# Kernel tuning notes

Measured on AMD Instinct MI355X. Metric: run time of the kernel, lower is better.

The kernel has to match this reference:

```python
import jax, jax.numpy as jnp
import numpy as np

DIM, HEADS, DHEAD = 256, 8, 64
INNER = HEADS * DHEAD
EPS = 1e-5


def _ln(x, g, b):
    m = x.mean(-1, keepdims=True)
    v = ((x - m) ** 2).mean(-1, keepdims=True)
    return (x - m) / jnp.sqrt(v + EPS) * g + b


def setup_inputs() -> dict:
    key = jax.random.key(0)
    ks = jax.random.split(key, 24)
    b, n, Q, K = 1, 6, 900, 1408
    d = DIM
    s = lambda fan_in: 1.0 / np.sqrt(fan_in)
    inp = {
        "k_g": jax.random.normal(ks[0], (b, n, K, d), jnp.float32),
        "q_g": jax.random.normal(ks[1], (b, n, Q, d), jnp.float32),
        "k_a": jax.random.normal(ks[2], (b, n, K, d), jnp.float32),
        "q_a": jax.random.normal(ks[3], (b, Q, d), jnp.float32),
        "v": jax.random.normal(ks[4], (b, n, K, d), jnp.float32),
        "mask": jax.random.randint(ks[5], (b, n, K), 0, 2).astype(bool),
        # projections (stored as (in, out))
        "W_qg": jax.random.uniform(ks[6], (d, INNER), jnp.float32, -s(d), s(d)),
        "b_qg": jnp.zeros((INNER,), jnp.float32),
        "W_kg": jax.random.uniform(ks[7], (d, INNER), jnp.float32, -s(d), s(d)),
        "b_kg": jnp.zeros((INNER,), jnp.float32),
        "W_qa": jax.random.uniform(ks[8], (d, INNER), jnp.float32, -s(d), s(d)),
        "b_qa": jnp.zeros((INNER,), jnp.float32),
        "W_ka": jax.random.uniform(ks[9], (d, INNER), jnp.float32, -s(d), s(d)),
        "b_ka": jnp.zeros((INNER,), jnp.float32),
        "W_v": jax.random.uniform(ks[10], (d, INNER), jnp.float32, -s(d), s(d)),
        "b_v": jnp.zeros((INNER,), jnp.float32),
        "W_o": jax.random.uniform(ks[11], (INNER, d), jnp.float32, -s(INNER), s(INNER)),
        "b_o": jnp.zeros((d,), jnp.float32),
        "ln1_g": jnp.ones((d,), jnp.float32),
        "ln1_b": jnp.zeros((d,), jnp.float32),
        "W_m1": jax.random.uniform(ks[12], (d, 2 * d), jnp.float32, -s(d), s(d)),
        "b_m1": jnp.zeros((2 * d,), jnp.float32),
        "W_m2": jax.random.uniform(ks[13], (2 * d, d), jnp.float32, -s(2 * d), s(2 * d)),
        "b_m2": jnp.zeros((d,), jnp.float32),
        "ln2_g": jnp.ones((d,), jnp.float32),
        "ln2_b": jnp.zeros((d,), jnp.float32),
        "scale_g": jnp.full((HEADS,), DHEAD ** -0.5, jnp.float32),
        "scale_a": jnp.full((HEADS,), DHEAD ** -0.5, jnp.float32),
    }
    return inp


def reference(k_g, q_g, k_a, q_a, v, mask,
              W_qg, b_qg, W_kg, b_kg, W_qa, b_qa, W_ka, b_ka, W_v, b_v,
              W_o, b_o, ln1_g, ln1_b, W_m1, b_m1, W_m2, b_m2, ln2_g, ln2_b,
              scale_g, scale_a):
    b, n, Q, _ = q_g.shape
    K = k_g.shape[2]
    h, dh = HEADS, DHEAD
    skip = q_a

    def split(x):  # (..., h*dh) -> (b, h, ..., dh)
        return jnp.moveaxis(x.reshape(x.shape[:-1] + (h, dh)), -2, 1)

    kg = split(k_g @ W_kg + b_kg)          # (b, h, n, K, dh)
    qg = split(q_g @ W_qg + b_qg)          # (b, h, n, Q, dh)
    ka = split(k_a @ W_ka + b_ka)          # (b, h, n, K, dh)
    qa = split(q_a @ W_qa + b_qa)          # (b, h, Q, dh)
    vv = split(v @ W_v + b_v)              # (b, h, n, K, dh)

    dot_g = jnp.einsum('bhnqd,bhnkd->bhnqk', qg, kg)
    dot_a = jnp.einsum('bhqd,bhnkd->bhnqk', qa, ka)
    sg = scale_g[None, :, None, None, None]
    sa = scale_a[None, :, None, None, None]
    dot = sg * dot_g + sa * dot_a
    dot = jnp.where(mask[:, None, :, None, :], -jnp.inf, dot)

    # softmax jointly over (n, K)
    dot = dot.transpose(0, 1, 3, 2, 4).reshape(b, h, Q, n * K)
    att = jax.nn.softmax(dot, axis=-1)
    vflat = vv.reshape(b, h, n * K, dh)
    a = jnp.einsum('bhqk,bhkd->bhqd', att, vflat)
    a = a.transpose(0, 2, 1, 3).reshape(b, Q, h * dh)

    z = a @ W_o + b_o + skip
    z = _ln(z, ln1_g, ln1_b)
    z = z + (jax.nn.gelu(z @ W_m1 + b_m1, approximate=False) @ W_m2 + b_m2)
    z = _ln(z, ln2_g, ln2_b)
    return z
```

## Files before the change

### kernel.cpp

```cpp
#include <hip/hip_runtime.h>
#include <stdint.h>

typedef unsigned short u16;
typedef _Float16 half8 __attribute__((ext_vector_type(8)));
typedef _Float16 half4 __attribute__((ext_vector_type(4)));
typedef _Float16 half2 __attribute__((ext_vector_type(2)));
typedef float f32x4 __attribute__((ext_vector_type(4)));

__device__ __forceinline__ u16 f2h(float f) {
    _Float16 h = (_Float16)f; u16 u; __builtin_memcpy(&u, &h, 2); return u;
}
__device__ __forceinline__ float h2f(u16 u) {
    _Float16 h; __builtin_memcpy(&h, &u, 2); return (float)h;
}

template<int CTRL>
__device__ __forceinline__ float dppf(float x) {
    return __builtin_bit_cast(float,
        __builtin_amdgcn_update_dpp(0, __builtin_bit_cast(int, x), CTRL, 0xF, 0xF, false));
}
__device__ __forceinline__ float sum16(float x) {
    x += dppf<0xB1>(x);
    x += dppf<0x4E>(x);
    x += dppf<0x124>(x);
    x += dppf<0x128>(x);
    return x;
}

__global__ __launch_bounds__(256) void prep_kernel(
    const float* __restrict__ W_qg, const float* __restrict__ W_kg,
    const float* __restrict__ W_qa, const float* __restrict__ W_ka,
    const float* __restrict__ W_v,  const float* __restrict__ W_o,
    const float* __restrict__ W_m1, const float* __restrict__ W_m2,
    u16* __restrict__ T_qg, u16* __restrict__ T_kg, u16* __restrict__ T_qa,
    u16* __restrict__ T_ka, u16* __restrict__ T_v,  u16* __restrict__ T_o,
    u16* __restrict__ T_m1, u16* __restrict__ T_m2,
    const float* __restrict__ scale_g, const float* __restrict__ scale_a,
    const float* __restrict__ b_kg, const float* __restrict__ b_ka,
    float* __restrict__ bkg_s, float* __restrict__ bka_s,
    const int* __restrict__ mask, int* __restrict__ mflag)
{
    const int z = blockIdx.z;
    const int tid = threadIdx.x;
    if (z == 8) {
        if (blockIdx.y != 0) return;
        if (blockIdx.x == 0) {
            __shared__ int f;
            if (tid == 0) f = 0;
            __syncthreads();
            int local = 0;
            for (int i = tid; i < 2112; i += 256) { int vv = mask[i]; if (vv & ~1) local = 1; }
            if (local) atomicOr(&f, 1);
            __syncthreads();
            if (tid == 0) *mflag = f;
        } else if (blockIdx.x == 1) {
            for (int j = tid; j < 512; j += 256) {
                bkg_s[j] = b_kg[j] * scale_g[j >> 6];
                bka_s[j] = b_ka[j] * scale_a[j >> 6];
            }
        }
        return;
    }
    const int K = (z == 5 || z == 7) ? 512 : 256;
    const int N = (z == 5 || z == 7) ? 256 : 512;
    const int k0 = blockIdx.x * 64, n0 = blockIdx.y * 64;
    if (k0 >= K || n0 >= N) return;
    const float* W = z==0?W_qg: z==1?W_kg: z==2?W_qa: z==3?W_ka: z==4?W_v: z==5?W_o: z==6?W_m1: W_m2;
    u16* D        = z==0?T_qg: z==1?T_kg: z==2?T_qa: z==3?T_ka: z==4?T_v: z==5?T_o: z==6?T_m1: T_m2;
    const float* scp = z==1 ? scale_g : z==3 ? scale_a : nullptr;

    __shared__ u16 T[64][80];
    const int cr = tid >> 4, cc = (tid & 15) * 4;
    const float sc = scp ? scp[(n0 + cc) >> 6] : 1.0f;
    #pragma unroll
    for (int i = 0; i < 4; ++i) {
        const int r = cr + i * 16;
        const float4 vv = *(const float4*)(W + (size_t)(k0 + r) * N + n0 + cc);
        T[cc + 0][r] = f2h(vv.x * sc);
        T[cc + 1][r] = f2h(vv.y * sc);
        T[cc + 2][r] = f2h(vv.z * sc);
        T[cc + 3][r] = f2h(vv.w * sc);
    }
    __syncthreads();
    const int nr = tid >> 2, part = (tid & 3) * 16;
    u16* drow = D + (size_t)(n0 + nr) * K + k0 + part;
    *(half8*)(drow)     = *(const half8*)&T[nr][part];
    *(half8*)(drow + 8) = *(const half8*)&T[nr][part + 8];
}

__global__ __launch_bounds__(256, 4) void proj_all(
    const float* __restrict__ k_g, const float* __restrict__ k_a,
    const float* __restrict__ v,   const float* __restrict__ q_g,
    const float* __restrict__ q_a,
    const u16* __restrict__ T_kg, const u16* __restrict__ T_ka,
    const u16* __restrict__ T_v,  const u16* __restrict__ T_qg,
    const u16* __restrict__ T_qa,
    const float* __restrict__ bkg_s, const float* __restrict__ bka_s,
    const float* __restrict__ b_v,   const float* __restrict__ b_qg,
    const float* __restrict__ b_qa,
    u16* __restrict__ qcat, u16* __restrict__ kcat, u16* __restrict__ vt)
{
    __shared__ u16 Ws[256 * 36];

    int bx = blockIdx.x;
    int mode, M;
    const float* X; const u16* Wt; const float* bias; u16* out;
    if (bx < 132)      { mode = 2; M = 8448; X = k_g; Wt = T_kg; bias = bkg_s; out = kcat; }
    else if (bx < 264) { mode = 3; M = 8448; X = k_a; Wt = T_ka; bias = bka_s; out = kcat; bx -= 132; }
    else if (bx < 396) { mode = 4; M = 8448; X = v;   Wt = T_v;  bias = b_v;   out = vt;   bx -= 264; }
    else if (bx < 481) { mode = 0; M = 5400; X = q_g; Wt = T_qg; bias = b_qg;  out = qcat; bx -= 396; }
    else               { mode = 1; M = 900;  X = q_a; Wt = T_qa; bias = b_qa;  out = qcat; bx -= 481; }
    const int rows_per_n = (mode == 0) ? 900 : 1408;

    const int tid = threadIdx.x;
    const int w = tid >> 6, lane = tid & 63;
    const int l15 = lane & 15, quad = lane >> 4;
    const int m0 = bx * 64;
    const int nbase = blockIdx.y * 256;
    const int row = m0 + w * 16 + l15;

    const float* xrow = X + (size_t)(row < M ? row : 0) * 256 + quad * 8;
    const u16* wcol = Wt + ((size_t)(nbase + tid) << 8);

    f32x4 o[4][4];
    #pragma unroll
    for (int nt = 0; nt < 4; ++nt)
        #pragma unroll
        for (int t = 0; t < 4; ++t) { o[nt][t][0]=0.f; o[nt][t][1]=0.f; o[nt][t][2]=0.f; o[nt][t][3]=0.f; }

    for (int k0 = 0; k0 < 8; ++k0) {
        {
            const uint4 w0 = *(const uint4*)(wcol + k0 * 32 + 0);
            const uint4 w1 = *(const uint4*)(wcol + k0 * 32 + 8);
            const uint4 w2 = *(const uint4*)(wcol + k0 * 32 + 16);
            const uint4 w3 = *(const uint4*)(wcol + k0 * 32 + 24);
            *(uint4*)&Ws[tid * 36 + 0]  = w0;
            *(uint4*)&Ws[tid * 36 + 8]  = w1;
            *(uint4*)&Ws[tid * 36 + 16] = w2;
            *(uint4*)&Ws[tid * 36 + 24] = w3;
        }
        __syncthreads();

        const float4 a0 = *(const float4*)(xrow + k0 * 32);
        const float4 a1 = *(const float4*)(xrow + k0 * 32 + 4);
        half8 af;
        af[0]=(_Float16)a0.x; af[1]=(_Float16)a0.y; af[2]=(_Float16)a0.z; af[3]=(_Float16)a0.w;
        af[4]=(_Float16)a1.x; af[5]=(_Float16)a1.y; af[6]=(_Float16)a1.z; af[7]=(_Float16)a1.w;

        #pragma unroll
        for (int nt = 0; nt < 4; ++nt)
            #pragma unroll
            for (int t = 0; t < 4; ++t) {
                const half8 bf = *(const half8*)&Ws[(nt * 64 + t * 16 + l15) * 36 + quad * 8];
                o[nt][t] = __builtin_amdgcn_mfma_f32_16x16x32_f16(af, bf, o[nt][t], 0, 0, 0);
            }
        __syncthreads();
    }

    #pragma unroll
    for (int nt = 0; nt < 4; ++nt) {
        const int n0 = nbase + nt * 64;
        const int hh = n0 >> 6;
        float bj[4];
        #pragma unroll
        for (int t = 0; t < 4; ++t) bj[t] = bias[n0 + t * 16 + l15];

        if (mode == 4) {
            const int gr0 = m0 + w * 16 + quad * 4;
            if (gr0 < M) {
                const int nI = gr0 / rows_per_n;
                const int rr = gr0 - nI * rows_per_n;
                u16* vb = out + (size_t)(hh * 6 + nI) * 64 * 1408;
                #pragma unroll
                for (int t = 0; t < 4; ++t) {
                    const int d = t * 16 + l15;
                    ushort4 pk;
                    pk.x = f2h(o[nt][t][0] + bj[t]);
                    pk.y = f2h(o[nt][t][1] + bj[t]);
                    pk.z = f2h(o[nt][t][2] + bj[t]);
                    pk.w = f2h(o[nt][t][3] + bj[t]);
                    *(ushort4*)&vb[(size_t)d * 1408 + rr] = pk;
                }
            }
        } else if (mode == 1) {
            #pragma unroll
            for (int r = 0; r < 4; ++r) {
                const int gr = m0 + w * 16 + quad * 4 + r;
                if (gr < M) {
                    for (int nb = 0; nb < 6; ++nb) {
                        u16* qb = out + (((size_t)(hh * 6 + nb) * 900 + gr) << 7) + 64;
                        #pragma unroll
                        for (int t = 0; t < 4; ++t)
                            qb[t * 16 + l15] = f2h(o[nt][t][r] + bj[t]);
                    }
                }
            }
        } else {
            const size_t kdim = (mode == 0) ? 900 : 1408;
            const int doff = (mode == 3) ? 64 : 0;
            #pragma unroll
            for (int r = 0; r < 4; ++r) {
                const int gr = m0 + w * 16 + quad * 4 + r;
                if (gr < M) {
                    const int nI = gr / rows_per_n;
                    const int rr = gr - nI * rows_per_n;
                    u16* ob = out + (((size_t)(hh * 6 + nI) * kdim + rr) << 7) + doff;
                    #pragma unroll
                    for (int t = 0; t < 4; ++t)
                        ob[t * 16 + l15] = f2h(o[nt][t][r] + bj[t]);
                }
            }
        }
    }
}

__global__ __launch_bounds__(256, 2) void attn_kernel(
    const u16* __restrict__ qcat, const u16* __restrict__ kcat,
    const u16* __restrict__ vt, const void* __restrict__ maskp,
    const int* __restrict__ mflag,
    u16* __restrict__ Opart, float* __restrict__ lpart)
{
    __shared__ __align__(16) u16 SMEM[64 * 136 + 64 * 72];
    __shared__ float Mb[64];
    u16* Ks = SMEM;
    u16* Vs = SMEM + 64 * 136;

    const int flat = blockIdx.x;
    const int hn_i = (flat & 7) + 8 * ((flat >> 3) % 6);
    const int qt = flat / 48;
    const int n = hn_i - (hn_i / 6) * 6;

    const int q0 = qt * 64;
    const int tid = threadIdx.x;
    const int w = tid >> 6, lane = tid & 63;
    const int l15 = lane & 15, quad = lane >> 4;
    const bool m8 = (*mflag != 0);
    const size_t hn = (size_t)hn_i;

    const u16* kbase = kcat + ((hn * 1408) << 7);
    const u16* vbase = vt + hn * 64 * 1408;
    const unsigned char* mB = (const unsigned char*)maskp;
    const int* mI = (const int*)maskp;
    const int mko = n * 1408;

    const int krow_s = tid >> 4;
    const int kcol_s = (tid & 15) * 8;
    const int vrow_s = tid >> 3;
    const int vcol_s = (tid & 7) * 8;

    half8 qf[4][4];
    #pragma unroll
    for (int qq = 0; qq < 4; ++qq) {
        const int gq = q0 + qq * 16 + l15;
        if (gq < 900) {
            const u16* qrow = qcat + ((hn * 900 + gq) << 7) + quad * 8;
            #pragma unroll
            for (int k0 = 0; k0 < 4; ++k0)
                qf[qq][k0] = *(const half8*)(qrow + k0 * 32);
        } else {
            #pragma unroll
            for (int k0 = 0; k0 < 4; ++k0)
                #pragma unroll
                for (int j = 0; j < 8; ++j) qf[qq][k0][j] = (_Float16)0.0f;
        }
    }

    f32x4 o[4][4];
    float lacc[4];
    #pragma unroll
    for (int dt = 0; dt < 4; ++dt)
        #pragma unroll
        for (int qq = 0; qq < 4; ++qq) { o[dt][qq][0]=0.f; o[dt][qq][1]=0.f; o[dt][qq][2]=0.f; o[dt][qq][3]=0.f; }
    #pragma unroll
    for (int qq = 0; qq < 4; ++qq) lacc[qq] = 0.f;

    uint4 kA, kB, kC, kD, vA, vB;
    float mreg = 0.0f;
    {
        kA = *(const uint4*)(kbase + ((size_t)( 0 + krow_s) << 7) + kcol_s);
        kB = *(const uint4*)(kbase + ((size_t)(16 + krow_s) << 7) + kcol_s);
        kC = *(const uint4*)(kbase + ((size_t)(32 + krow_s) << 7) + kcol_s);
        kD = *(const uint4*)(kbase + ((size_t)(48 + krow_s) << 7) + kcol_s);
        vA = *(const uint4*)(vbase + (size_t)(vrow_s)      * 1408 + vcol_s);
        vB = *(const uint4*)(vbase + (size_t)(32 + vrow_s) * 1408 + vcol_s);
        if (tid < 64) {
            const int ki = mko + tid;
            const int mv = m8 ? (int)mB[ki] : mI[ki];
            mreg = mv ? -1e30f : 0.0f;
        }
    }

    for (int cc = 0; cc < 22; ++cc) {
        *(uint4*)&Ks[( 0 + krow_s) * 136 + kcol_s] = kA;
        *(uint4*)&Ks[(16 + krow_s) * 136 + kcol_s] = kB;
        *(uint4*)&Ks[(32 + krow_s) * 136 + kcol_s] = kC;
        *(uint4*)&Ks[(48 + krow_s) * 136 + kcol_s] = kD;
        *(uint4*)&Vs[(vrow_s)      * 72 + vcol_s] = vA;
        *(uint4*)&Vs[(32 + vrow_s) * 72 + vcol_s] = vB;
        if (tid < 64) Mb[tid] = mreg;
        __syncthreads();

        if (cc < 21) {
            const int k0n = (cc + 1) * 64;
            kA = *(const uint4*)(kbase + ((size_t)(k0n +  0 + krow_s) << 7) + kcol_s);
            kB = *(const uint4*)(kbase + ((size_t)(k0n + 16 + krow_s) << 7) + kcol_s);
            kC = *(const uint4*)(kbase + ((size_t)(k0n + 32 + krow_s) << 7) + kcol_s);
            kD = *(const uint4*)(kbase + ((size_t)(k0n + 48 + krow_s) << 7) + kcol_s);
            vA = *(const uint4*)(vbase + (size_t)(vrow_s)      * 1408 + k0n + vcol_s);
            vB = *(const uint4*)(vbase + (size_t)(32 + vrow_s) * 1408 + k0n + vcol_s);
            if (tid < 64) {
                const int ki = mko + k0n + tid;
                const int mv = m8 ? (int)mB[ki] : mI[ki];
                mreg = mv ? -1e30f : 0.0f;
            }
        }

        float mb[4];
        #pragma unroll
        for (int r = 0; r < 4; ++r) mb[r] = Mb[w * 16 + quad * 4 + r];

        f32x4 s[4];
        #pragma unroll
        for (int qq = 0; qq < 4; ++qq) { s[qq][0]=mb[0]; s[qq][1]=mb[1]; s[qq][2]=mb[2]; s[qq][3]=mb[3]; }

        #pragma unroll
        for (int k0 = 0; k0 < 4; ++k0) {
            const half8 kf = *(const half8*)&Ks[(w * 16 + l15) * 136 + k0 * 32 + quad * 8];
            #pragma unroll
            for (int qq = 0; qq < 4; ++qq)
                s[qq] = __builtin_amdgcn_mfma_f32_16x16x32_f16(kf, qf[qq][k0], s[qq], 0, 0, 0);
        }

        half4 pf[4];
        #pragma unroll
        for (int qq = 0; qq < 4; ++qq) {
            const float p0 = __expf(s[qq][0]);
            const float p1 = __expf(s[qq][1]);
            const float p2 = __expf(s[qq][2]);
            const float p3 = __expf(s[qq][3]);
            lacc[qq] += (p0 + p1) + (p2 + p3);
            const half2 lo = __builtin_bit_cast(half2, __builtin_amdgcn_cvt_pkrtz(p0, p1));
            const half2 hi = __builtin_bit_cast(half2, __builtin_amdgcn_cvt_pkrtz(p2, p3));
            half4 pk; pk[0]=lo[0]; pk[1]=lo[1]; pk[2]=hi[0]; pk[3]=hi[1];
            pf[qq] = pk;
        }

        #pragma unroll
        for (int dt = 0; dt < 4; ++dt) {
            const half4 vf = *(const half4*)&Vs[(dt * 16 + l15) * 72 + w * 16 + quad * 4];
            #pragma unroll
            for (int qq = 0; qq < 4; ++qq)
                o[dt][qq] = __builtin_amdgcn_mfma_f32_16x16x16f16(vf, pf[qq], o[dt][qq], 0, 0, 0);
        }
        __syncthreads();
    }

    __syncthreads();
    float* Red = (float*)SMEM;
    float* Lp  = (float*)(SMEM + 64 * 136);

    #pragma unroll
    for (int qq = 0; qq < 4; ++qq)
        Lp[(w * 4 + quad) * 64 + qq * 16 + l15] = lacc[qq];
    #pragma unroll
    for (int qq = 0; qq < 4; ++qq)
        #pragma unroll
        for (int r = 0; r < 4; ++r)
            Red[(w * 16 + quad * 4 + r) * 68 + qq * 16 + l15] = o[0][qq][r];
    __syncthreads();

    if (tid < 64) {
        float l = 0.f;
        #pragma unroll
        for (int i = 0; i < 16; ++i) l += Lp[i * 64 + tid];
        if (q0 + tid < 900) lpart[hn_i * 900 + q0 + tid] = l;
    }

    const int dloc = tid & 15, qgrp = tid >> 4;
    #pragma unroll
    for (int dt = 0; dt < 4; ++dt) {
        #pragma unroll
        for (int i = 0; i < 4; ++i) {
            const int q = qgrp * 4 + i;
            const float sum = Red[( 0 + dloc) * 68 + q] + Red[(16 + dloc) * 68 + q]
                            + Red[(32 + dloc) * 68 + q] + Red[(48 + dloc) * 68 + q];
            const int gq = q0 + q;
            if (gq < 900)
                Opart[((size_t)hn_i * 900 + gq) * 64 + dt * 16 + dloc] = f2h(sum);
        }
        if (dt < 3) {
            __syncthreads();
            #pragma unroll
            for (int qq = 0; qq < 4; ++qq)
                #pragma unroll
                for (int r = 0; r < 4; ++r)
                    Red[(w * 16 + quad * 4 + r) * 68 + qq * 16 + l15] = o[dt + 1][qq][r];
            __syncthreads();
        }
    }
}

__global__ __launch_bounds__(256) void combine_kernel(
    const u16* __restrict__ Opart, const float* __restrict__ lpart,
    u16* __restrict__ a16)
{
    const int g = blockIdx.x * 256 + threadIdx.x;
    const int h = g / 14400;
    const int r = g - h * 14400;
    const int q = r >> 4;
    const int d4 = (r & 15) * 4;
    float l = 0.f;
    float o0 = 0.f, o1 = 0.f, o2 = 0.f, o3 = 0.f;
    #pragma unroll
    for (int s = 0; s < 6; ++s) {
        const int p = h * 6 + s;
        l += lpart[p * 900 + q];
        const ushort4 t = *(const ushort4*)&Opart[((size_t)p * 900 + q) * 64 + d4];
        o0 += h2f(t.x); o1 += h2f(t.y); o2 += h2f(t.z); o3 += h2f(t.w);
    }
    const float inv = 1.0f / fmaxf(l, 1e-30f);
    ushort4 outp;
    outp.x = f2h(o0 * inv); outp.y = f2h(o1 * inv);
    outp.z = f2h(o2 * inv); outp.w = f2h(o3 * inv);
    *(ushort4*)&a16[(size_t)q * 512 + h * 64 + d4] = outp;
}

__global__ __launch_bounds__(256) void epi_mega(
    const u16* __restrict__ a16, const u16* __restrict__ T_o,
    const u16* __restrict__ T_m1, const u16* __restrict__ T_m2,
    const float* __restrict__ b_o, const float* __restrict__ q_a,
    const float* __restrict__ ln1_g, const float* __restrict__ ln1_b,
    const float* __restrict__ b_m1, const float* __restrict__ b_m2,
    const float* __restrict__ ln2_g, const float* __restrict__ ln2_b,
    float* __restrict__ outf)
{
    __shared__ u16 Z1[16][264];
    __shared__ u16 H[16][520];
    __shared__ float Ssum[4][16];
    __shared__ float Ssq[4][16];

    const int tid = threadIdx.x;
    const int w = tid >> 6, lane = tid & 63;
    const int l15 = lane & 15, quad = lane >> 4;
    const int m0 = blockIdx.x * 4;

    {
        const int ar = m0 + l15;
        const u16* arow = a16 + (size_t)(ar < 900 ? ar : 899) * 512 + quad * 8;

        f32x4 acc[4];
        #pragma unroll
        for (int t = 0; t < 4; ++t) { acc[t][0]=0.f; acc[t][1]=0.f; acc[t][2]=0.f; acc[t][3]=0.f; }

        #pragma unroll
        for (int k0 = 0; k0 < 16; ++k0) {
            const half8 af = *(const half8*)(arow + k0 * 32);
            #pragma unroll
            for (int t = 0; t < 4; ++t) {
                const int nn = w * 64 + t * 16 + l15;
                const half8 bf = *(const half8*)(T_o + (size_t)nn * 512 + k0 * 32 + quad * 8);
                acc[t] = __builtin_amdgcn_mfma_f32_16x16x32_f16(af, bf, acc[t], 0, 0, 0);
            }
        }

        float vals[4][4];
        #pragma unroll
        for (int r = 0; r < 4; ++r) {
            const int row = m0 + quad * 4 + r;
            const int rows = row < 900 ? row : 899;
            float s = 0.f, sq = 0.f;
            #pragma unroll
            for (int t = 0; t < 4; ++t) {
                const int col = w * 64 + t * 16 + l15;
                const float x = acc[t][r] + b_o[col] + q_a[(size_t)rows * 256 + col];
                vals[r][t] = x; s += x; sq += x * x;
            }
            s = sum16(s); sq = sum16(sq);
            if (l15 == 0) { Ssum[w][quad * 4 + r] = s; Ssq[w][quad * 4 + r] = sq; }
        }
        __syncthreads();

        #pragma unroll
        for (int r = 0; r < 4; ++r) {
            const int rl = quad * 4 + r;
            const float st = Ssum[0][rl] + Ssum[1][rl] + Ssum[2][rl] + Ssum[3][rl];
            const float qt = Ssq[0][rl] + Ssq[1][rl] + Ssq[2][rl] + Ssq[3][rl];
            const float mean = st * (1.0f / 256.0f);
            const float var  = qt * (1.0f / 256.0f) - mean * mean;
            const float inv  = rsqrtf(var + 1e-5f);
            #pragma unroll
            for (int t = 0; t < 4; ++t) {
                const int col = w * 64 + t * 16 + l15;
                const float z = (vals[r][t] - mean) * inv * ln1_g[col] + ln1_b[col];
                Z1[rl][col] = f2h(z);
            }
        }
        __syncthreads();
    }

    {
        f32x4 acc[8];
        #pragma unroll
        for (int t = 0; t < 8; ++t) { acc[t][0]=0.f; acc[t][1]=0.f; acc[t][2]=0.f; acc[t][3]=0.f; }

        #pragma unroll
        for (int k0 = 0; k0 < 8; ++k0) {
            const half8 af = *(const half8*)&Z1[l15][k0 * 32 + quad * 8];
            #pragma unroll
            for (int t = 0; t < 8; ++t) {
                const int nn = w * 128 + t * 16 + l15;
                const half8 bf = *(const half8*)(T_m1 + (size_t)nn * 256 + k0 * 32 + quad * 8);
                acc[t] = __builtin_amdgcn_mfma_f32_16x16x32_f16(af, bf, acc[t], 0, 0, 0);
            }
        }

        #pragma unroll
        for (int r = 0; r < 4; ++r) {
            const int rl = quad * 4 + r;
            #pragma unroll
            for (int t = 0; t < 8; ++t) {
                const int col = w * 128 + t * 16 + l15;
                const float x = acc[t][r] + b_m1[col];
                H[rl][col] = f2h(0.5f * x * (1.0f + erff(x * 0.70710678118654752f)));
            }
        }
        __syncthreads();
    }

    {
        f32x4 acc[4];
        #pragma unroll
        for (int t = 0; t < 4; ++t) { acc[t][0]=0.f; acc[t][1]=0.f; acc[t][2]=0.f; acc[t][3]=0.f; }

        #pragma unroll
        for (int k0 = 0; k0 < 16; ++k0) {
            const half8 af = *(const half8*)&H[l15][k0 * 32 + quad * 8];
            #pragma unroll
            for (int t = 0; t < 4; ++t) {
                const int nn = w * 64 + t * 16 + l15;
                const half8 bf = *(const half8*)(T_m2 + (size_t)nn * 512 + k0 * 32 + quad * 8);
                acc[t] = __builtin_amdgcn_mfma_f32_16x16x32_f16(af, bf, acc[t], 0, 0, 0);
            }
        }

        float vals[4][4];
        #pragma unroll
        for (int r = 0; r < 4; ++r) {
            const int rl = quad * 4 + r;
            float s = 0.f, sq = 0.f;
            #pragma unroll
            for (int t = 0; t < 4; ++t) {
                const int col = w * 64 + t * 16 + l15;
                const float x = acc[t][r] + b_m2[col] + h2f(Z1[rl][col]);
                vals[r][t] = x; s += x; sq += x * x;
            }
            s = sum16(s); sq = sum16(sq);
            if (l15 == 0) { Ssum[w][rl] = s; Ssq[w][rl] = sq; }
        }
        __syncthreads();

        #pragma unroll
        for (int r = 0; r < 4; ++r) {
            const int rl = quad * 4 + r;
            const float st = Ssum[0][rl] + Ssum[1][rl] + Ssum[2][rl] + Ssum[3][rl];
            const float qt = Ssq[0][rl] + Ssq[1][rl] + Ssq[2][rl] + Ssq[3][rl];
            const float mean = st * (1.0f / 256.0f);
            const float var  = qt * (1.0f / 256.0f) - mean * mean;
            const float inv  = rsqrtf(var + 1e-5f);
            const int row = m0 + rl;
            if (rl < 4 && row < 900) {
                #pragma unroll
                for (int t = 0; t < 4; ++t) {
                    const int col = w * 64 + t * 16 + l15;
                    outf[(size_t)row * 256 + col] = (vals[r][t] - mean) * inv * ln2_g[col] + ln2_b[col];
                }
            }
        }
    }
}

extern "C" void kernel_launch(void* const* d_in, const int* in_sizes, int n_in,
                              void* d_out, int out_size, void* d_ws, size_t ws_size,
                              hipStream_t stream)
{
    const float* k_g  = (const float*)d_in[0];
    const float* q_g  = (const float*)d_in[1];
    const float* k_a  = (const float*)d_in[2];
    const float* q_a  = (const float*)d_in[3];
    const float* v    = (const float*)d_in[4];
    const void*  mask = d_in[5];
    const float* W_qg = (const float*)d_in[6];
    const float* b_qg = (const float*)d_in[7];
    const float* W_kg = (const float*)d_in[8];
    const float* b_kg = (const float*)d_in[9];
    const float* W_qa = (const float*)d_in[10];
    const float* b_qa = (const float*)d_in[11];
    const float* W_ka = (const float*)d_in[12];
    const float* b_ka = (const float*)d_in[13];
    const float* W_v  = (const float*)d_in[14];
    const float* b_v  = (const float*)d_in[15];
    const float* W_o  = (const float*)d_in[16];
    const float* b_o  = (const float*)d_in[17];
    const float* ln1_g = (const float*)d_in[18];
    const float* ln1_b = (const float*)d_in[19];
    const float* W_m1 = (const float*)d_in[20];
    const float* b_m1 = (const float*)d_in[21];
    const float* W_m2 = (const float*)d_in[22];
    const float* b_m2 = (const float*)d_in[23];
    const float* ln2_g = (const float*)d_in[24];
    const float* ln2_b = (const float*)d_in[25];
    const float* scale_g = (const float*)d_in[26];
    const float* scale_a = (const float*)d_in[27];

    char* ws = (char*)d_ws;
    size_t off = 0;
    auto alloc = [&](size_t bytes) -> void* {
        void* p = ws + off;
        off += (bytes + 255) & ~(size_t)255;
        return p;
    };
    u16*   qcat  = (u16*)  alloc((size_t)8 * 6 * 900  * 128 * 2);
    u16*   kcat  = (u16*)  alloc((size_t)8 * 6 * 1408 * 128 * 2);
    u16*   vt    = (u16*)  alloc((size_t)8 * 6 * 64 * 1408 * 2);
    u16*   a16   = (u16*)  alloc((size_t)900 * 512 * 2);
    u16*   Tw[8];
    for (int i = 0; i < 8; ++i) Tw[i] = (u16*)alloc((size_t)512 * 256 * 2);
    float* bkg_s = (float*)alloc((size_t)512 * 4);
    float* bka_s = (float*)alloc((size_t)512 * 4);
    int*   mflag = (int*)  alloc(256);
    u16*   Opart = (u16*)  alloc((size_t)48 * 900 * 64 * 2);
    float* lpart = (float*)alloc((size_t)48 * 900 * 4);

    prep_kernel<<<dim3(8, 8, 9), 256, 0, stream>>>(
        W_qg, W_kg, W_qa, W_ka, W_v, W_o, W_m1, W_m2,
        Tw[0], Tw[1], Tw[2], Tw[3], Tw[4], Tw[5], Tw[6], Tw[7],
        scale_g, scale_a, b_kg, b_ka, bkg_s, bka_s, (const int*)mask, mflag);

    proj_all<<<dim3(496, 2), 256, 0, stream>>>(
        k_g, k_a, v, q_g, q_a,
        Tw[1], Tw[3], Tw[4], Tw[0], Tw[2],
        bkg_s, bka_s, b_v, b_qg, b_qa,
        qcat, kcat, vt);

    attn_kernel<<<720, 256, 0, stream>>>(qcat, kcat, vt, mask, mflag, Opart, lpart);
    combine_kernel<<<450, 256, 0, stream>>>(Opart, lpart, a16);

    epi_mega<<<225, 256, 0, stream>>>(
        a16, Tw[5], Tw[6], Tw[7],
        b_o, q_a, ln1_g, ln1_b, b_m1, b_m2, ln2_g, ln2_b,
        (float*)d_out);
}
```

Measured before the change: 256.9 us.

## Split attention keys in two, fuse combine into epilogue kernel

The attention kernel now splits the 1408-key range into two halves of 11 chunks each, doubling the grid to 1440 blocks and raising launch bounds to 4 blocks per SM, so partial outputs double to 96 slices. The separate combine kernel is removed, and its reduction over 12 partials (6 n x 2 splits) is folded into the start of epi_mega, which stages the normalized attention rows in shared memory. This aims to improve occupancy and GPU fill and to remove one launch plus an intermediate buffer round trip. The cost is more partial writes, and the tighter register budget may cause spills.

```diff
diff --git a/kernel.cpp b/kernel.cpp
--- a/kernel.cpp
+++ b/kernel.cpp
@@ -214,7 +214,7 @@
     }
 }
 
-__global__ __launch_bounds__(256, 2) void attn_kernel(
+__global__ __launch_bounds__(256, 4) void attn_kernel(
     const u16* __restrict__ qcat, const u16* __restrict__ kcat,
     const u16* __restrict__ vt, const void* __restrict__ maskp,
     const int* __restrict__ mflag,
@@ -226,8 +226,11 @@
     u16* Vs = SMEM + 64 * 136;
 
     const int flat = blockIdx.x;
-    const int hn_i = (flat & 7) + 8 * ((flat >> 3) % 6);
-    const int qt = flat / 48;
+    const int grp = flat >> 3;
+    const int qt = grp % 15;
+    const int rest = grp / 15;
+    const int hn_i = (flat & 7) + 8 * (rest % 6);
+    const int sp = rest / 6;
     const int n = hn_i - (hn_i / 6) * 6;
 
     const int q0 = qt * 64;
@@ -277,20 +280,21 @@
     uint4 kA, kB, kC, kD, vA, vB;
     float mreg = 0.0f;
     {
-        kA = *(const uint4*)(kbase + ((size_t)( 0 + krow_s) << 7) + kcol_s);
-        kB = *(const uint4*)(kbase + ((size_t)(16 + krow_s) << 7) + kcol_s);
-        kC = *(const uint4*)(kbase + ((size_t)(32 + krow_s) << 7) + kcol_s);
-        kD = *(const uint4*)(kbase + ((size_t)(48 + krow_s) << 7) + kcol_s);
-        vA = *(const uint4*)(vbase + (size_t)(vrow_s)      * 1408 + vcol_s);
-        vB = *(const uint4*)(vbase + (size_t)(32 + vrow_s) * 1408 + vcol_s);
+        const int k0c = sp * 11 * 64;
+        kA = *(const uint4*)(kbase + ((size_t)(k0c +  0 + krow_s) << 7) + kcol_s);
+        kB = *(const uint4*)(kbase + ((size_t)(k0c + 16 + krow_s) << 7) + kcol_s);
+        kC = *(const uint4*)(kbase + ((size_t)(k0c + 32 + krow_s) << 7) + kcol_s);
+        kD = *(const uint4*)(kbase + ((size_t)(k0c + 48 + krow_s) << 7) + kcol_s);
+        vA = *(const uint4*)(vbase + (size_t)(vrow_s)      * 1408 + k0c + vcol_s);
+        vB = *(const uint4*)(vbase + (size_t)(32 + vrow_s) * 1408 + k0c + vcol_s);
         if (tid < 64) {
-            const int ki = mko + tid;
+            const int ki = mko + k0c + tid;
             const int mv = m8 ? (int)mB[ki] : mI[ki];
             mreg = mv ? -1e30f : 0.0f;
         }
     }
 
-    for (int cc = 0; cc < 22; ++cc) {
+    for (int cc = 0; cc < 11; ++cc) {
         *(uint4*)&Ks[( 0 + krow_s) * 136 + kcol_s] = kA;
         *(uint4*)&Ks[(16 + krow_s) * 136 + kcol_s] = kB;
         *(uint4*)&Ks[(32 + krow_s) * 136 + kcol_s] = kC;
@@ -300,8 +304,8 @@
         if (tid < 64) Mb[tid] = mreg;
         __syncthreads();
 
-        if (cc < 21) {
-            const int k0n = (cc + 1) * 64;
+        if (cc < 10) {
+            const int k0n = (sp * 11 + cc + 1) * 64;
             kA = *(const uint4*)(kbase + ((size_t)(k0n +  0 + krow_s) << 7) + kcol_s);
             kB = *(const uint4*)(kbase + ((size_t)(k0n + 16 + krow_s) << 7) + kcol_s);
             kC = *(const uint4*)(kbase + ((size_t)(k0n + 32 + krow_s) << 7) + kcol_s);
@@ -369,11 +373,12 @@
             Red[(w * 16 + quad * 4 + r) * 68 + qq * 16 + l15] = o[0][qq][r];
     __syncthreads();
 
+    const int p = sp * 48 + hn_i;
     if (tid < 64) {
         float l = 0.f;
         #pragma unroll
         for (int i = 0; i < 16; ++i) l += Lp[i * 64 + tid];
-        if (q0 + tid < 900) lpart[hn_i * 900 + q0 + tid] = l;
+        if (q0 + tid < 900) lpart[p * 900 + q0 + tid] = l;
     }
 
     const int dloc = tid & 15, qgrp = tid >> 4;
@@ -386,7 +391,7 @@
                             + Red[(32 + dloc) * 68 + q] + Red[(48 + dloc) * 68 + q];
             const int gq = q0 + q;
             if (gq < 900)
-                Opart[((size_t)hn_i * 900 + gq) * 64 + dt * 16 + dloc] = f2h(sum);
+                Opart[((size_t)p * 900 + gq) * 64 + dt * 16 + dloc] = f2h(sum);
         }
         if (dt < 3) {
             __syncthreads();
@@ -400,33 +405,9 @@
     }
 }
 
-__global__ __launch_bounds__(256) void combine_kernel(
+__global__ __launch_bounds__(256) void epi_mega(
     const u16* __restrict__ Opart, const float* __restrict__ lpart,
-    u16* __restrict__ a16)
-{
-    const int g = blockIdx.x * 256 + threadIdx.x;
-    const int h = g / 14400;
-    const int r = g - h * 14400;
-    const int q = r >> 4;
-    const int d4 = (r & 15) * 4;
-    float l = 0.f;
-    float o0 = 0.f, o1 = 0.f, o2 = 0.f, o3 = 0.f;
-    #pragma unroll
-    for (int s = 0; s < 6; ++s) {
-        const int p = h * 6 + s;
-        l += lpart[p * 900 + q];
-        const ushort4 t = *(const ushort4*)&Opart[((size_t)p * 900 + q) * 64 + d4];
-        o0 += h2f(t.x); o1 += h2f(t.y); o2 += h2f(t.z); o3 += h2f(t.w);
-    }
-    const float inv = 1.0f / fmaxf(l, 1e-30f);
-    ushort4 outp;
-    outp.x = f2h(o0 * inv); outp.y = f2h(o1 * inv);
-    outp.z = f2h(o2 * inv); outp.w = f2h(o3 * inv);
-    *(ushort4*)&a16[(size_t)q * 512 + h * 64 + d4] = outp;
-}
-
-__global__ __launch_bounds__(256) void epi_mega(
-    const u16* __restrict__ a16, const u16* __restrict__ T_o,
+    const u16* __restrict__ T_o,
     const u16* __restrict__ T_m1, const u16* __restrict__ T_m2,
     const float* __restrict__ b_o, const float* __restrict__ q_a,
     const float* __restrict__ ln1_g, const float* __restrict__ ln1_b,
@@ -434,6 +415,7 @@
     const float* __restrict__ ln2_g, const float* __restrict__ ln2_b,
     float* __restrict__ outf)
 {
+    __shared__ u16 A16[4][520];
     __shared__ u16 Z1[16][264];
     __shared__ u16 H[16][520];
     __shared__ float Ssum[4][16];
@@ -445,16 +427,41 @@
     const int m0 = blockIdx.x * 4;
 
     {
-        const int ar = m0 + l15;
-        const u16* arow = a16 + (size_t)(ar < 900 ? ar : 899) * 512 + quad * 8;
-
+        const int r = tid >> 6;
+        const int cg = tid & 63;
+        const int c8 = cg * 8;
+        const int hh = cg >> 3;
+        const int d8 = c8 & 56;
+        const int q = m0 + r;
+        float l = 0.f;
+        float a0=0.f,a1=0.f,a2=0.f,a3=0.f,a4=0.f,a5=0.f,a6=0.f,a7=0.f;
+        #pragma unroll
+        for (int s = 0; s < 12; ++s) {
+            const int p = ((s & 1) ? 48 : 0) + hh * 6 + (s >> 1);
+            l += lpart[p * 900 + q];
+            const u16* ob = Opart + ((size_t)p * 900 + q) * 64 + d8;
+            const ushort4 t0 = *(const ushort4*)ob;
+            const ushort4 t1 = *(const ushort4*)(ob + 4);
+            a0 += h2f(t0.x); a1 += h2f(t0.y); a2 += h2f(t0.z); a3 += h2f(t0.w);
+            a4 += h2f(t1.x); a5 += h2f(t1.y); a6 += h2f(t1.z); a7 += h2f(t1.w);
+        }
+        const float inv = 1.0f / fmaxf(l, 1e-30f);
+        ushort4 o0, o1;
+        o0.x = f2h(a0 * inv); o0.y = f2h(a1 * inv); o0.z = f2h(a2 * inv); o0.w = f2h(a3 * inv);
+        o1.x = f2h(a4 * inv); o1.y = f2h(a5 * inv); o1.z = f2h(a6 * inv); o1.w = f2h(a7 * inv);
+        *(ushort4*)&A16[r][c8]     = o0;
+        *(ushort4*)&A16[r][c8 + 4] = o1;
+    }
+    __syncthreads();
+
+    {
         f32x4 acc[4];
         #pragma unroll
         for (int t = 0; t < 4; ++t) { acc[t][0]=0.f; acc[t][1]=0.f; acc[t][2]=0.f; acc[t][3]=0.f; }
 
         #pragma unroll
         for (int k0 = 0; k0 < 16; ++k0) {
-            const half8 af = *(const half8*)(arow + k0 * 32);
+            const half8 af = *(const half8*)&A16[l15 & 3][k0 * 32 + quad * 8];
             #pragma unroll
             for (int t = 0; t < 4; ++t) {
                 const int nn = w * 64 + t * 16 + l15;
@@ -466,13 +473,12 @@
         float vals[4][4];
         #pragma unroll
         for (int r = 0; r < 4; ++r) {
-            const int row = m0 + quad * 4 + r;
-            const int rows = row < 900 ? row : 899;
+            const int row = m0 + ((quad * 4 + r) & 3);
             float s = 0.f, sq = 0.f;
             #pragma unroll
             for (int t = 0; t < 4; ++t) {
                 const int col = w * 64 + t * 16 + l15;
-                const float x = acc[t][r] + b_o[col] + q_a[(size_t)rows * 256 + col];
+                const float x = acc[t][r] + b_o[col] + q_a[(size_t)row * 256 + col];
                 vals[r][t] = x; s += x; sq += x * x;
             }
             s = sum16(s); sq = sum16(sq);
@@ -622,14 +628,13 @@
     u16*   qcat  = (u16*)  alloc((size_t)8 * 6 * 900  * 128 * 2);
     u16*   kcat  = (u16*)  alloc((size_t)8 * 6 * 1408 * 128 * 2);
     u16*   vt    = (u16*)  alloc((size_t)8 * 6 * 64 * 1408 * 2);
-    u16*   a16   = (u16*)  alloc((size_t)900 * 512 * 2);
     u16*   Tw[8];
     for (int i = 0; i < 8; ++i) Tw[i] = (u16*)alloc((size_t)512 * 256 * 2);
     float* bkg_s = (float*)alloc((size_t)512 * 4);
     float* bka_s = (float*)alloc((size_t)512 * 4);
     int*   mflag = (int*)  alloc(256);
-    u16*   Opart = (u16*)  alloc((size_t)48 * 900 * 64 * 2);
-    float* lpart = (float*)alloc((size_t)48 * 900 * 4);
+    u16*   Opart = (u16*)  alloc((size_t)96 * 900 * 64 * 2);
+    float* lpart = (float*)alloc((size_t)96 * 900 * 4);
 
     prep_kernel<<<dim3(8, 8, 9), 256, 0, stream>>>(
         W_qg, W_kg, W_qa, W_ka, W_v, W_o, W_m1, W_m2,
@@ -642,11 +647,10 @@
         bkg_s, bka_s, b_v, b_qg, b_qa,
         qcat, kcat, vt);
 
-    attn_kernel<<<720, 256, 0, stream>>>(qcat, kcat, vt, mask, mflag, Opart, lpart);
-    combine_kernel<<<450, 256, 0, stream>>>(Opart, lpart, a16);
+    attn_kernel<<<1440, 256, 0, stream>>>(qcat, kcat, vt, mask, mflag, Opart, lpart);
 
     epi_mega<<<225, 256, 0, stream>>>(
-        a16, Tw[5], Tw[6], Tw[7],
+        Opart, lpart, Tw[5], Tw[6], Tw[7],
         b_o, q_a, ln1_g, ln1_b, b_m1, b_m2, ln2_g, ln2_b,
         (float*)d_out);
 }
```

Result: slower. 417.3 us (+62.4%).
